# Kernel tuning notes

Measured on AMD Instinct MI355X. Metric: run time of the kernel, lower is better.

The kernel has to match this reference:

```python
import jax, jax.numpy as jnp
import numpy as np

B, S, D_MODEL, HEADS = 4, 2048, 1024, 16
D_HEAD = D_MODEL // HEADS  # 64


def setup_inputs() -> dict:
    key = jax.random.key(0)
    ks = jax.random.split(key, 10)
    scale = 1.0 / np.sqrt(D_MODEL)
    return {
        "query": jax.random.normal(ks[0], (B, S, D_MODEL), dtype=jnp.float32),
        "key_": jax.random.normal(ks[1], (B, S, D_MODEL), dtype=jnp.float32),
        "value": jax.random.normal(ks[2], (B, S, D_MODEL), dtype=jnp.float32),
        "mask": jax.random.randint(ks[3], (B, S, S), 0, 2).astype(bool),
        "Wq": jax.random.normal(ks[4], (D_MODEL, HEADS, D_HEAD), dtype=jnp.float32) * scale,
        "bq": jnp.zeros((HEADS, D_HEAD), dtype=jnp.float32),
        "Wk": jax.random.normal(ks[5], (D_MODEL, HEADS, D_HEAD), dtype=jnp.float32) * scale,
        "bk": jnp.zeros((HEADS, D_HEAD), dtype=jnp.float32),
        "Wv": jax.random.normal(ks[6], (D_MODEL, HEADS, D_HEAD), dtype=jnp.float32) * scale,
        "bv": jnp.zeros((HEADS, D_HEAD), dtype=jnp.float32),
        "Wo": jax.random.normal(ks[7], (HEADS, D_HEAD, D_MODEL), dtype=jnp.float32) * (1.0 / np.sqrt(D_MODEL)),
        "bo": jnp.zeros((D_MODEL,), dtype=jnp.float32),
    }


def reference(query, key_, value, mask, Wq, bq, Wk, bk, Wv, bv, Wo, bo):
    # MakeHead: linear projection to (B, heads, S, d_head)
    q = jnp.einsum("bse,ehd->bhsd", query, Wq) + bq[:, None, :]
    k = jnp.einsum("bse,ehd->bhsd", key_, Wk) + bk[:, None, :]
    v = jnp.einsum("bse,ehd->bhsd", value, Wv) + bv[:, None, :]

    # dot_product_attention (note: module divides by sqrt(d_head) AFTER softmax@V)
    logits = jnp.einsum("bhsd,bhtd->bhst", q, k)  # [B,H,S,S]
    logits = jnp.where(mask[:, None, :, :], jnp.float32(-1e8), logits)
    score = jax.nn.softmax(logits, axis=-1)
    attn = jnp.einsum("bhst,bhtd->bhsd", score, v) / jnp.sqrt(jnp.float32(D_HEAD))

    # MergeHeads: project back to d_output = d_model
    out = jnp.einsum("bhsd,hdo->bso", attn, Wo) + bo
    return out
```

## Files before the change

### kernel.cpp

```cpp
#include <hip/hip_runtime.h>

typedef _Float16 h16;
typedef h16 half8 __attribute__((ext_vector_type(8)));
typedef h16 half4v __attribute__((ext_vector_type(4)));
typedef float f32x4 __attribute__((ext_vector_type(4)));

#define BB 4
#define SS 2048
#define EE 1024
#define HH 16
#define DH 64

__device__ __forceinline__ void gload_lds16(const void* g, void* l) {
  __builtin_amdgcn_global_load_lds((const __attribute__((address_space(1))) void*)g,
                                   (__attribute__((address_space(3))) void*)l, 16, 0, 0);
}

__global__ __launch_bounds__(256) void mha_pack_mask(const int* __restrict__ mask,
                                                     unsigned* __restrict__ maskw) {
  int gid = blockIdx.x * 256 + threadIdx.x;
  unsigned long long bal = __ballot(mask[gid] != 0);
  int lane = threadIdx.x & 63;
  if (lane == 0) maskw[gid >> 5] = (unsigned)bal;
  else if (lane == 32) maskw[gid >> 5] = (unsigned)(bal >> 32);
}

__global__ __launch_bounds__(256) void mha_wtrans(const float* __restrict__ w0, const float* __restrict__ w1,
                                                  const float* __restrict__ w2, const float* __restrict__ w3,
                                                  h16* __restrict__ o0, h16* __restrict__ o1,
                                                  h16* __restrict__ o2, h16* __restrict__ o3) {
  __shared__ float t[32][33];
  int z = blockIdx.z;
  const float* src = z == 0 ? w0 : z == 1 ? w1 : z == 2 ? w2 : w3;
  h16* dst = z == 0 ? o0 : z == 1 ? o1 : z == 2 ? o2 : o3;
  int x = threadIdx.x, y = threadIdx.y;
  int bx = blockIdx.x * 32, by = blockIdx.y * 32;
#pragma unroll
  for (int i = 0; i < 4; ++i)
    t[y + i * 8][x] = src[(size_t)(by + y + i * 8) * EE + bx + x];
  __syncthreads();
#pragma unroll
  for (int i = 0; i < 4; ++i)
    dst[(size_t)(bx + y + i * 8) * EE + by + x] = (h16)t[x][y + i * 8];
}

__global__ __launch_bounds__(256) void mha_cvt(const float* __restrict__ s0, const float* __restrict__ s1,
                                               const float* __restrict__ s2, h16* __restrict__ d0,
                                               h16* __restrict__ d1, h16* __restrict__ d2) {
  int z = blockIdx.z;
  const float* s = z == 0 ? s0 : z == 1 ? s1 : s2;
  h16* d = z == 0 ? d0 : z == 1 ? d1 : d2;
  size_t i = ((size_t)blockIdx.x * 256 + threadIdx.x) * 8;
  float4 a = *reinterpret_cast<const float4*>(&s[i]);
  float4 b = *reinterpret_cast<const float4*>(&s[i + 4]);
  half8 h;
  h[0] = (h16)a.x; h[1] = (h16)a.y; h[2] = (h16)a.z; h[3] = (h16)a.w;
  h[4] = (h16)b.x; h[5] = (h16)b.y; h[6] = (h16)b.z; h[7] = (h16)b.w;
  *reinterpret_cast<half8*>(&d[i]) = h;
}

#define PTM 128
#define PTN 128
#define PBK 32

__global__ __launch_bounds__(256) void mha_proj(
    const h16* __restrict__ Xq, const h16* __restrict__ Xk, const h16* __restrict__ Xv,
    const h16* __restrict__ Wqt, const h16* __restrict__ Wkt, const h16* __restrict__ Wvt,
    const float* __restrict__ bq, const float* __restrict__ bk, const float* __restrict__ bv,
    h16* __restrict__ Oq, h16* __restrict__ Ok, h16* __restrict__ Ov) {
  int z = blockIdx.z;
  const h16* X = z == 0 ? Xq : z == 1 ? Xk : Xv;
  const h16* Wt = z == 0 ? Wqt : z == 1 ? Wkt : Wvt;
  const float* bias = z == 0 ? bq : z == 1 ? bk : bv;
  h16* out = z == 0 ? Oq : z == 1 ? Ok : Ov;

  __shared__ __align__(16) h16 As[PTM * PBK];
  __shared__ __align__(16) h16 Bs[PTN * PBK];

  int tid = threadIdx.x;
  int lane = tid & 63, wid = tid >> 6;
  int l15 = lane & 15, l4 = lane >> 4;
  int wr = wid >> 1, wc = wid & 1;
  int mbase = blockIdx.y * PTM;
  int nbase = blockIdx.x * PTN;

  const f32x4 fz = {0.f, 0.f, 0.f, 0.f};
  f32x4 acc[4][4];
#pragma unroll
  for (int i = 0; i < 4; ++i)
#pragma unroll
    for (int j = 0; j < 4; ++j) acc[i][j] = fz;

  int row0 = wid * 32 + (lane >> 2), chunk = lane & 3;

  for (int kt = 0; kt < EE; kt += PBK) {
#pragma unroll
    for (int c = 0; c < 2; ++c) {
      int r = row0 + c * 16;
      gload_lds16(&X[(size_t)(mbase + r) * EE + kt + chunk * 8], &As[wid * 1024 + c * 512]);
      gload_lds16(&Wt[(size_t)(nbase + r) * EE + kt + chunk * 8], &Bs[wid * 1024 + c * 512]);
    }
    __syncthreads();

    half8 a[4], bfr[4];
#pragma unroll
    for (int i = 0; i < 4; ++i) {
      a[i] = *reinterpret_cast<const half8*>(&As[(wr * 64 + i * 16 + l15) * PBK + l4 * 8]);
      bfr[i] = *reinterpret_cast<const half8*>(&Bs[(wc * 64 + i * 16 + l15) * PBK + l4 * 8]);
    }
#pragma unroll
    for (int mi = 0; mi < 4; ++mi)
#pragma unroll
      for (int ni = 0; ni < 4; ++ni)
        acc[mi][ni] = __builtin_amdgcn_mfma_f32_16x16x32_f16(a[mi], bfr[ni], acc[mi][ni], 0, 0, 0);
    __syncthreads();
  }

  const float qscale = (z == 0) ? 1.44269504088896f : 1.0f;
#pragma unroll
  for (int mi = 0; mi < 4; ++mi) {
#pragma unroll
    for (int ni = 0; ni < 4; ++ni) {
      int n = nbase + wc * 64 + ni * 16 + l15;
      float bv_ = bias[n];
      int h = n >> 6, d = n & 63;
#pragma unroll
      for (int j = 0; j < 4; ++j) {
        int m = mbase + wr * 64 + mi * 16 + l4 * 4 + j;
        int b_ = m >> 11, s = m & 2047;
        h16 hv = (h16)((acc[mi][ni][j] + bv_) * qscale);
        if (z != 2)
          out[(((size_t)(b_ * HH + h)) * SS + s) * DH + d] = hv;
        else
          out[(((size_t)(b_ * HH + h)) * DH + d) * SS + s] = hv;
      }
    }
  }
}

__global__ __launch_bounds__(256) void mha_attn(
    const h16* __restrict__ qh, const h16* __restrict__ kh, const h16* __restrict__ vh,
    const unsigned* __restrict__ maskw, h16* __restrict__ ah) {
  __shared__ __align__(16) h16 Ks[2][64 * 64];
  __shared__ __align__(16) h16 Vs[2][64 * 64];
  __shared__ __align__(16) h16 Ps[4][32 * 64];
  __shared__ uint4 MaskLut[16];

  int bh = blockIdx.y;
  int b_ = bh >> 4, hh = bh & 15;
  int tid = threadIdx.x, lane = tid & 63, wid = tid >> 6;
  int l15 = lane & 15, l4 = lane >> 4;

  if (tid < 16) {
    unsigned n = tid;
    MaskLut[n] = make_uint4((n & 1) ? 0u : ~0u, (n & 2) ? 0u : ~0u,
                            (n & 4) ? 0u : ~0u, (n & 8) ? 0u : ~0u);
  }

  const h16* Qb = qh + (size_t)bh * SS * DH;
  const h16* Kb = kh + (size_t)bh * SS * DH;
  const h16* Vb = vh + (size_t)bh * DH * SS;
  int qrow0 = blockIdx.x * 128 + wid * 32;

  half8 qf[2][2];
#pragma unroll
  for (int mi = 0; mi < 2; ++mi)
#pragma unroll
    for (int kk = 0; kk < 2; ++kk)
      qf[mi][kk] = *reinterpret_cast<const half8*>(&Qb[(size_t)(qrow0 + mi * 16 + l15) * DH + kk * 32 + l4 * 8]);

  float m_run[2] = {-1e30f, -1e30f};
  f32x4 l_vec[2];
  f32x4 oacc[2][4];
  const f32x4 fz = {0.f, 0.f, 0.f, 0.f};
#pragma unroll
  for (int mi = 0; mi < 2; ++mi) {
    l_vec[mi] = fz;
#pragma unroll
    for (int di = 0; di < 4; ++di) oacc[mi][di] = fz;
  }

  const unsigned* mwb = maskw + ((size_t)b_ * SS + qrow0) * 64;

  int srow = wid * 16 + (lane >> 3);
  int schunk = lane & 7;
  int sh0 = l4 * 4;

#pragma unroll
  for (int c = 0; c < 2; ++c) {
    int r = srow + c * 8;
    int gk = schunk ^ (r & 7);
    gload_lds16(&Kb[(size_t)r * DH + gk * 8], &Ks[0][wid * 1024 + c * 512]);
    gload_lds16(&Vb[(size_t)r * SS + gk * 8], &Vs[0][wid * 1024 + c * 512]);
  }
  unsigned mw[2][2];
  mw[0][0] = mwb[l15 * 64 + 0];
  mw[0][1] = mwb[l15 * 64 + 1];
  mw[1][0] = mwb[(16 + l15) * 64 + 0];
  mw[1][1] = mwb[(16 + l15) * 64 + 1];
  __syncthreads();

  const unsigned negb = __float_as_uint(-1e5f);

  h16* Pw = &Ps[wid][0];
  int it = 0;
  for (int tt = 0; tt < SS; tt += 64, it ^= 1) {
    unsigned mwn[2][2] = {{0u, 0u}, {0u, 0u}};
    if (tt + 64 < SS) {
#pragma unroll
      for (int c = 0; c < 2; ++c) {
        int r = srow + c * 8;
        int gk = schunk ^ (r & 7);
        gload_lds16(&Kb[(size_t)(tt + 64 + r) * DH + gk * 8], &Ks[it ^ 1][wid * 1024 + c * 512]);
        gload_lds16(&Vb[(size_t)r * SS + tt + 64 + gk * 8], &Vs[it ^ 1][wid * 1024 + c * 512]);
      }
      int tw = (tt + 64) >> 5;
      mwn[0][0] = mwb[l15 * 64 + tw];
      mwn[0][1] = mwb[l15 * 64 + tw + 1];
      mwn[1][0] = mwb[(16 + l15) * 64 + tw];
      mwn[1][1] = mwb[(16 + l15) * 64 + tw + 1];
    }

    const h16* Kt = &Ks[it][0];
    half8 kf[4][2];
#pragma unroll
    for (int ni = 0; ni < 4; ++ni) {
      int trow = ni * 16 + l15;
      int sw = trow & 7;
      kf[ni][0] = *reinterpret_cast<const half8*>(&Kt[trow * 64 + (l4 ^ sw) * 8]);
      kf[ni][1] = *reinterpret_cast<const half8*>(&Kt[trow * 64 + ((4 + l4) ^ sw) * 8]);
    }
    f32x4 st[2][4];
    __builtin_amdgcn_s_setprio(1);
#pragma unroll
    for (int mi = 0; mi < 2; ++mi)
#pragma unroll
      for (int ni = 0; ni < 4; ++ni) {
        f32x4 t_ = fz;
        t_ = __builtin_amdgcn_mfma_f32_16x16x32_f16(kf[ni][0], qf[mi][0], t_, 0, 0, 0);
        t_ = __builtin_amdgcn_mfma_f32_16x16x32_f16(kf[ni][1], qf[mi][1], t_, 0, 0, 0);
        st[mi][ni] = t_;
      }
    __builtin_amdgcn_s_setprio(0);

#pragma unroll
    for (int mi = 0; mi < 2; ++mi) {
#pragma unroll
      for (int ni = 0; ni < 4; ++ni) {
        unsigned nib = (mw[mi][ni >> 1] >> (sh0 + 16 * (ni & 1))) & 15u;
        uint4 mm = MaskLut[nib];
        st[mi][ni][0] = __uint_as_float((mm.x & __float_as_uint(st[mi][ni][0])) | (~mm.x & negb));
        st[mi][ni][1] = __uint_as_float((mm.y & __float_as_uint(st[mi][ni][1])) | (~mm.y & negb));
        st[mi][ni][2] = __uint_as_float((mm.z & __float_as_uint(st[mi][ni][2])) | (~mm.z & negb));
        st[mi][ni][3] = __uint_as_float((mm.w & __float_as_uint(st[mi][ni][3])) | (~mm.w & negb));
      }
    }

#pragma unroll
    for (int mi = 0; mi < 2; ++mi) {
      float t0 = fmaxf(fmaxf(st[mi][0][0], st[mi][0][1]), st[mi][0][2]);
      float t1 = fmaxf(fmaxf(st[mi][0][3], st[mi][1][0]), st[mi][1][1]);
      float t2 = fmaxf(fmaxf(st[mi][1][2], st[mi][1][3]), st[mi][2][0]);
      float t3 = fmaxf(fmaxf(st[mi][2][1], st[mi][2][2]), st[mi][2][3]);
      float t4 = fmaxf(fmaxf(st[mi][3][0], st[mi][3][1]), st[mi][3][2]);
      float tmax = fmaxf(fmaxf(fmaxf(t0, t1), fmaxf(t2, t3)), fmaxf(t4, st[mi][3][3]));
      tmax = fmaxf(tmax, __shfl_xor(tmax, 16));
      tmax = fmaxf(tmax, __shfl_xor(tmax, 32));
      if (!__all(tmax - m_run[mi] <= 8.0f)) {
        float mnew = fmaxf(m_run[mi], tmax);
        float sc = __builtin_amdgcn_exp2f(m_run[mi] - mnew);
        l_vec[mi] *= sc;
#pragma unroll
        for (int di = 0; di < 4; ++di) oacc[mi][di] *= sc;
        m_run[mi] = mnew;
      }
      float mneg = -m_run[mi];
#pragma unroll
      for (int ni = 0; ni < 4; ++ni)
#pragma unroll
        for (int j = 0; j < 4; ++j)
          st[mi][ni][j] = __builtin_amdgcn_exp2f(st[mi][ni][j] + mneg);
      l_vec[mi] += (st[mi][0] + st[mi][1]) + (st[mi][2] + st[mi][3]);
    }

#pragma unroll
    for (int mi = 0; mi < 2; ++mi) {
      int q = mi * 16 + l15;
#pragma unroll
      for (int ni = 0; ni < 4; ++ni) {
        auto pa = __builtin_amdgcn_cvt_pkrtz(st[mi][ni][0], st[mi][ni][1]);
        auto pb = __builtin_amdgcn_cvt_pkrtz(st[mi][ni][2], st[mi][ni][3]);
        half4v w;
        w[0] = pa[0]; w[1] = pa[1]; w[2] = pb[0]; w[3] = pb[1];
        int c16 = (ni * 2 + (l4 >> 1)) ^ (q & 7);
        *reinterpret_cast<half4v*>(&Pw[q * 64 + c16 * 8 + (l4 & 1) * 4]) = w;
      }
    }

    const h16* Vt = &Vs[it][0];
    half8 vf[4][2], pf[2][2];
#pragma unroll
    for (int di = 0; di < 4; ++di) {
      int dr = di * 16 + l15, sw = dr & 7;
      vf[di][0] = *reinterpret_cast<const half8*>(&Vt[dr * 64 + (l4 ^ sw) * 8]);
      vf[di][1] = *reinterpret_cast<const half8*>(&Vt[dr * 64 + ((4 + l4) ^ sw) * 8]);
    }
#pragma unroll
    for (int mi = 0; mi < 2; ++mi) {
      int q = mi * 16 + l15;
      pf[mi][0] = *reinterpret_cast<const half8*>(&Pw[q * 64 + ((l4 ^ (q & 7)) * 8)]);
      pf[mi][1] = *reinterpret_cast<const half8*>(&Pw[q * 64 + (((4 + l4) ^ (q & 7)) * 8)]);
    }
    __builtin_amdgcn_s_setprio(1);
#pragma unroll
    for (int mi = 0; mi < 2; ++mi)
#pragma unroll
      for (int di = 0; di < 4; ++di) {
        oacc[mi][di] = __builtin_amdgcn_mfma_f32_16x16x32_f16(vf[di][0], pf[mi][0], oacc[mi][di], 0, 0, 0);
        oacc[mi][di] = __builtin_amdgcn_mfma_f32_16x16x32_f16(vf[di][1], pf[mi][1], oacc[mi][di], 0, 0, 0);
      }
    __builtin_amdgcn_s_setprio(0);

    mw[0][0] = mwn[0][0]; mw[0][1] = mwn[0][1];
    mw[1][0] = mwn[1][0]; mw[1][1] = mwn[1][1];
    __syncthreads();
  }

#pragma unroll
  for (int mi = 0; mi < 2; ++mi) {
    float l = (l_vec[mi][0] + l_vec[mi][1]) + (l_vec[mi][2] + l_vec[mi][3]);
    l += __shfl_xor(l, 16);
    l += __shfl_xor(l, 32);
    float inv = 1.f / (l * 8.f);
    size_t rowb = ((size_t)b_ * SS + (qrow0 + mi * 16 + l15)) * EE + hh * DH;
#pragma unroll
    for (int di = 0; di < 4; ++di) {
      half4v w;
#pragma unroll
      for (int j = 0; j < 4; ++j) w[j] = (h16)(oacc[mi][di][j] * inv);
      *reinterpret_cast<half4v*>(&ah[rowb + di * 16 + l4 * 4]) = w;
    }
  }
}

__global__ __launch_bounds__(256) void mha_oproj(
    const h16* __restrict__ A, const h16* __restrict__ Wot,
    const float* __restrict__ bo, float* __restrict__ out) {
  __shared__ __align__(16) h16 As[PTM * PBK];
  __shared__ __align__(16) h16 Bs[PTN * PBK];
  int tid = threadIdx.x, lane = tid & 63, wid = tid >> 6;
  int l15 = lane & 15, l4 = lane >> 4;
  int wr = wid >> 1, wc = wid & 1;
  int mbase = blockIdx.y * PTM, nbase = blockIdx.x * PTN;
  const f32x4 fz = {0.f, 0.f, 0.f, 0.f};
  f32x4 acc[4][4];
#pragma unroll
  for (int i = 0; i < 4; ++i)
#pragma unroll
    for (int j = 0; j < 4; ++j) acc[i][j] = fz;
  int row0 = wid * 32 + (lane >> 2), chunk = lane & 3;
  for (int kt = 0; kt < EE; kt += PBK) {
#pragma unroll
    for (int c = 0; c < 2; ++c) {
      int r = row0 + c * 16;
      gload_lds16(&A[(size_t)(mbase + r) * EE + kt + chunk * 8], &As[wid * 1024 + c * 512]);
      gload_lds16(&Wot[(size_t)(nbase + r) * EE + kt + chunk * 8], &Bs[wid * 1024 + c * 512]);
    }
    __syncthreads();
    half8 a[4], bfr[4];
#pragma unroll
    for (int i = 0; i < 4; ++i) {
      a[i] = *reinterpret_cast<const half8*>(&As[(wr * 64 + i * 16 + l15) * PBK + l4 * 8]);
      bfr[i] = *reinterpret_cast<const half8*>(&Bs[(wc * 64 + i * 16 + l15) * PBK + l4 * 8]);
    }
#pragma unroll
    for (int mi = 0; mi < 4; ++mi)
#pragma unroll
      for (int ni = 0; ni < 4; ++ni)
        acc[mi][ni] = __builtin_amdgcn_mfma_f32_16x16x32_f16(a[mi], bfr[ni], acc[mi][ni], 0, 0, 0);
    __syncthreads();
  }
#pragma unroll
  for (int mi = 0; mi < 4; ++mi)
#pragma unroll
    for (int ni = 0; ni < 4; ++ni) {
      int n = nbase + wc * 64 + ni * 16 + l15;
      float bb = bo[n];
#pragma unroll
      for (int j = 0; j < 4; ++j) {
        int m = mbase + wr * 64 + mi * 16 + l4 * 4 + j;
        out[(size_t)m * EE + n] = acc[mi][ni][j] + bb;
      }
    }
}

extern "C" void kernel_launch(void* const* d_in, const int* in_sizes, int n_in,
                              void* d_out, int out_size, void* d_ws, size_t ws_size,
                              hipStream_t stream) {
  const float* query = (const float*)d_in[0];
  const float* key_ = (const float*)d_in[1];
  const float* value = (const float*)d_in[2];
  const int* mask = (const int*)d_in[3];
  const float* Wq = (const float*)d_in[4];
  const float* bq = (const float*)d_in[5];
  const float* Wk = (const float*)d_in[6];
  const float* bk = (const float*)d_in[7];
  const float* Wv = (const float*)d_in[8];
  const float* bv = (const float*)d_in[9];
  const float* Wo = (const float*)d_in[10];
  const float* bo = (const float*)d_in[11];
  float* out = (float*)d_out;

  const size_t MH = 1u << 20;
  const size_t QH = (size_t)BB * HH * SS * DH;
  h16* wqt = (h16*)d_ws;
  h16* wkt = wqt + MH;
  h16* wvt = wkt + MH;
  h16* wot = wvt + MH;
  h16* qh = wot + MH;
  h16* kh = qh + QH;
  h16* vh = kh + QH;
  h16* ah = vh + QH;
  unsigned* maskw = (unsigned*)(ah + QH);

  h16* xq = ah;
  h16* xk = (h16*)d_out;
  h16* xv = xk + QH;

  mha_pack_mask<<<(BB * SS * SS) / 256, 256, 0, stream>>>(mask, maskw);
  mha_wtrans<<<dim3(32, 32, 4), dim3(32, 8), 0, stream>>>(Wq, Wk, Wv, Wo, wqt, wkt, wvt, wot);
  mha_cvt<<<dim3((BB * SS * EE) / 2048, 1, 3), 256, 0, stream>>>(query, key_, value, xq, xk, xv);
  mha_proj<<<dim3(EE / PTN, (BB * SS) / PTM, 3), 256, 0, stream>>>(
      xq, xk, xv, wqt, wkt, wvt, bq, bk, bv, qh, kh, vh);
  mha_attn<<<dim3(SS / 128, BB * HH), 256, 0, stream>>>(qh, kh, vh, maskw, ah);
  mha_oproj<<<dim3(EE / PTN, (BB * SS) / PTM), 256, 0, stream>>>(ah, wot, bo, out);
}
```

Baseline: 328.0 us.

## Keep P in registers and use 16x16x16 MFMA for PV

Removes the per-wave LDS round trip for the softmax probabilities. The S-tile accumulator layout from the QK MFMA is reused directly as the B operand of a 16x16x16 f16 MFMA, with V fragments loaded as matching half4 chunks. The mask lookup table in LDS is replaced with per-bit shift-and-sign selects computed in registers. The trade is twice as many smaller MFMA instructions, each with lower per-instruction throughput, plus more V LDS loads, in exchange for dropping the P stores and loads and the LUT reads.

```diff
diff --git a/kernel.cpp b/kernel.cpp
--- a/kernel.cpp
+++ b/kernel.cpp
@@ -143,19 +143,12 @@
     const unsigned* __restrict__ maskw, h16* __restrict__ ah) {
   __shared__ __align__(16) h16 Ks[2][64 * 64];
   __shared__ __align__(16) h16 Vs[2][64 * 64];
-  __shared__ __align__(16) h16 Ps[4][32 * 64];
-  __shared__ uint4 MaskLut[16];
 
   int bh = blockIdx.y;
   int b_ = bh >> 4, hh = bh & 15;
   int tid = threadIdx.x, lane = tid & 63, wid = tid >> 6;
   int l15 = lane & 15, l4 = lane >> 4;
-
-  if (tid < 16) {
-    unsigned n = tid;
-    MaskLut[n] = make_uint4((n & 1) ? 0u : ~0u, (n & 2) ? 0u : ~0u,
-                            (n & 4) ? 0u : ~0u, (n & 8) ? 0u : ~0u);
-  }
+  int l4h = l4 >> 1, l4l = l4 & 1;
 
   const h16* Qb = qh + (size_t)bh * SS * DH;
   const h16* Kb = kh + (size_t)bh * SS * DH;
@@ -202,7 +195,6 @@
 
   const unsigned negb = __float_as_uint(-1e5f);
 
-  h16* Pw = &Ps[wid][0];
   int it = 0;
   for (int tt = 0; tt < SS; tt += 64, it ^= 1) {
     unsigned mwn[2][2] = {{0u, 0u}, {0u, 0u}};
@@ -243,19 +235,32 @@
       }
     __builtin_amdgcn_s_setprio(0);
 
+    const h16* Vt = &Vs[it][0];
+    half4v vf16[4][4];
+#pragma unroll
+    for (int di = 0; di < 4; ++di) {
+      int dr = di * 16 + l15, sw = dr & 7;
+#pragma unroll
+      for (int ni = 0; ni < 4; ++ni) {
+        int ch = (ni * 2 + l4h) ^ sw;
+        vf16[di][ni] = *reinterpret_cast<const half4v*>(&Vt[dr * 64 + ch * 8 + l4l * 4]);
+      }
+    }
+
 #pragma unroll
     for (int mi = 0; mi < 2; ++mi) {
 #pragma unroll
       for (int ni = 0; ni < 4; ++ni) {
-        unsigned nib = (mw[mi][ni >> 1] >> (sh0 + 16 * (ni & 1))) & 15u;
-        uint4 mm = MaskLut[nib];
-        st[mi][ni][0] = __uint_as_float((mm.x & __float_as_uint(st[mi][ni][0])) | (~mm.x & negb));
-        st[mi][ni][1] = __uint_as_float((mm.y & __float_as_uint(st[mi][ni][1])) | (~mm.y & negb));
-        st[mi][ni][2] = __uint_as_float((mm.z & __float_as_uint(st[mi][ni][2])) | (~mm.z & negb));
-        st[mi][ni][3] = __uint_as_float((mm.w & __float_as_uint(st[mi][ni][3])) | (~mm.w & negb));
-      }
-    }
-
+        unsigned m4 = mw[mi][ni >> 1] >> (sh0 + 16 * (ni & 1));
+#pragma unroll
+        for (int j = 0; j < 4; ++j) {
+          unsigned sel = (unsigned)(((int)(m4 << (31 - j))) >> 31);
+          st[mi][ni][j] = __uint_as_float((~sel & __float_as_uint(st[mi][ni][j])) | (sel & negb));
+        }
+      }
+    }
+
+    half4v pfrag[2][4];
 #pragma unroll
     for (int mi = 0; mi < 2; ++mi) {
       float t0 = fmaxf(fmaxf(st[mi][0][0], st[mi][0][1]), st[mi][0][2]);
@@ -281,44 +286,23 @@
         for (int j = 0; j < 4; ++j)
           st[mi][ni][j] = __builtin_amdgcn_exp2f(st[mi][ni][j] + mneg);
       l_vec[mi] += (st[mi][0] + st[mi][1]) + (st[mi][2] + st[mi][3]);
-    }
-
-#pragma unroll
-    for (int mi = 0; mi < 2; ++mi) {
-      int q = mi * 16 + l15;
 #pragma unroll
       for (int ni = 0; ni < 4; ++ni) {
         auto pa = __builtin_amdgcn_cvt_pkrtz(st[mi][ni][0], st[mi][ni][1]);
         auto pb = __builtin_amdgcn_cvt_pkrtz(st[mi][ni][2], st[mi][ni][3]);
-        half4v w;
-        w[0] = pa[0]; w[1] = pa[1]; w[2] = pb[0]; w[3] = pb[1];
-        int c16 = (ni * 2 + (l4 >> 1)) ^ (q & 7);
-        *reinterpret_cast<half4v*>(&Pw[q * 64 + c16 * 8 + (l4 & 1) * 4]) = w;
-      }
-    }
-
-    const h16* Vt = &Vs[it][0];
-    half8 vf[4][2], pf[2][2];
-#pragma unroll
-    for (int di = 0; di < 4; ++di) {
-      int dr = di * 16 + l15, sw = dr & 7;
-      vf[di][0] = *reinterpret_cast<const half8*>(&Vt[dr * 64 + (l4 ^ sw) * 8]);
-      vf[di][1] = *reinterpret_cast<const half8*>(&Vt[dr * 64 + ((4 + l4) ^ sw) * 8]);
-    }
-#pragma unroll
-    for (int mi = 0; mi < 2; ++mi) {
-      int q = mi * 16 + l15;
-      pf[mi][0] = *reinterpret_cast<const half8*>(&Pw[q * 64 + ((l4 ^ (q & 7)) * 8)]);
-      pf[mi][1] = *reinterpret_cast<const half8*>(&Pw[q * 64 + (((4 + l4) ^ (q & 7)) * 8)]);
-    }
+        pfrag[mi][ni][0] = pa[0]; pfrag[mi][ni][1] = pa[1];
+        pfrag[mi][ni][2] = pb[0]; pfrag[mi][ni][3] = pb[1];
+      }
+    }
+
     __builtin_amdgcn_s_setprio(1);
 #pragma unroll
     for (int mi = 0; mi < 2; ++mi)
 #pragma unroll
-      for (int di = 0; di < 4; ++di) {
-        oacc[mi][di] = __builtin_amdgcn_mfma_f32_16x16x32_f16(vf[di][0], pf[mi][0], oacc[mi][di], 0, 0, 0);
-        oacc[mi][di] = __builtin_amdgcn_mfma_f32_16x16x32_f16(vf[di][1], pf[mi][1], oacc[mi][di], 0, 0, 0);
-      }
+      for (int di = 0; di < 4; ++di)
+#pragma unroll
+        for (int ni = 0; ni < 4; ++ni)
+          oacc[mi][di] = __builtin_amdgcn_mfma_f32_16x16x16f16(vf16[di][ni], pfrag[mi][ni], oacc[mi][di], 0, 0, 0);
     __builtin_amdgcn_s_setprio(0);
 
     mw[0][0] = mwn[0][0]; mw[0][1] = mwn[0][1];
```

Measured after the change: 339.9 us. 1.04x slower.
